# Optimization experiments

Measured on AMD Instinct MI355X. Metric: run time of the kernel, lower is better.

The kernel has to match this reference:

```python
import jax, jax.numpy as jnp
import numpy as np

N, E, D_IN, D_OUT, R = 50000, 800000, 128, 128, 8


def setup_inputs() -> dict:
    key = jax.random.key(0)
    ks = jax.random.split(key, 6)
    x = jax.random.normal(ks[0], (N, D_IN), dtype=jnp.float32)
    W_rel = jax.random.normal(ks[1], (R, D_IN, D_OUT), dtype=jnp.float32) * (1.0 / np.sqrt(D_IN))
    W_self_w = jax.random.normal(ks[2], (D_OUT, D_IN), dtype=jnp.float32) * (1.0 / np.sqrt(D_IN))
    W_self_b = jax.random.normal(ks[3], (D_OUT,), dtype=jnp.float32) * 0.01
    edge_index = jax.random.randint(ks[4], (2, E), 0, N, dtype=jnp.int32)
    edge_type = jax.random.randint(ks[5], (E,), 0, R, dtype=jnp.int32)
    return {"x": x, "W_rel": W_rel, "W_self_w": W_self_w, "W_self_b": W_self_b,
            "edge_index": edge_index, "edge_type": edge_type}


def reference(x, W_rel, W_self_w, W_self_b, edge_index, edge_type):
    n = x.shape[0]
    # self-loop linear (nn.Linear: y = x @ W.T + b)
    out = x @ W_self_w.T + W_self_b
    src = edge_index[0]
    dst = edge_index[1]
    # Per-relation transform of all nodes: h[r, n, :] = x[n] @ W_rel[r]
    # (mathematically identical to per-edge bmm(x[src], W_rel[rel]))
    h = jnp.einsum('nd,rdo->rno', x, W_rel)  # [R, N, D_OUT]
    msg = h[edge_type, src]                   # [E, D_OUT] gather
    agg = jax.ops.segment_sum(msg, dst, num_segments=n)  # scatter-add
    deg = jax.ops.segment_sum(jnp.ones_like(dst, dtype=x.dtype), dst, num_segments=n)
    deg = jnp.maximum(deg, 1.0)[:, None]
    out = jax.nn.relu(out + agg / deg)
    # dropout p=0.0 / eval mode -> identity
    return out
```

## Files before the change

### kernel.cpp

```cpp
#include <hip/hip_runtime.h>
#include <hip/hip_bf16.h>


#define D 128
#define RNUM 8
#define KREL (RNUM * D)
#define KTOT (KREL + D)
#define BLK_M 64

#define BSHIFT 6
#define BRANGE 64
#define BCAP   2048
#define NBKT_MAX 784
#define CSTRIDE 16

typedef short short8 __attribute__((ext_vector_type(8)));
typedef float float4v __attribute__((ext_vector_type(4)));
typedef float float2v __attribute__((ext_vector_type(2)));

static __device__ __forceinline__ unsigned int f2b(float f) {
    unsigned int u = __float_as_uint(f);
    return (u + 0x7fffu + ((u >> 16) & 1u)) >> 16;
}
static __device__ __forceinline__ float b2f_lo(unsigned int u) {
    return __uint_as_float(u << 16);
}
static __device__ __forceinline__ float b2f_hi(unsigned int u) {
    return __uint_as_float(u & 0xffff0000u);
}

static __device__ __forceinline__ void gl_lds16(const void* g, void* l) {
    __builtin_amdgcn_global_load_lds(
        (const __attribute__((address_space(1))) unsigned int*)g,
        (__attribute__((address_space(3))) unsigned int*)l, 16, 0, 0);
}

__global__ void prep_kernel(const float* __restrict__ x,
                            const float* __restrict__ W_rel,
                            const float* __restrict__ W_self,
                            unsigned short* __restrict__ xb,
                            unsigned short* __restrict__ Bt,
                            int* __restrict__ gcur,
                            int Nn, int xb_blocks, int bt_blocks, int gz) {
    if (blockIdx.x < (unsigned)xb_blocks) {
        int t = blockIdx.x * 256 + threadIdx.x;
        int n = t >> 5;
        int c = (t & 31) * 4;
        if (n >= Nn) return;
        float4 v = *(const float4*)(x + (size_t)n * D + c);
        unsigned int p0 = f2b(v.x) | (f2b(v.y) << 16);
        unsigned int p1 = f2b(v.z) | (f2b(v.w) << 16);
        *(uint2*)(xb + (size_t)n * D + c) = make_uint2(p0, p1);
    } else if (blockIdx.x < (unsigned)(xb_blocks + bt_blocks)) {
        int idx = (blockIdx.x - xb_blocks) * 256 + threadIdx.x;
        if (idx >= 128 * KTOT) return;
        int o = idx / KTOT;
        int k = idx - o * KTOT;
        float v = (k < KREL) ? W_rel[(size_t)k * D + o]
                             : W_self[(size_t)o * D + (k - KREL)];
        Bt[idx] = (unsigned short)f2b(v);
    } else {
        int idx = (blockIdx.x - xb_blocks - bt_blocks) * 256 + threadIdx.x;
        if (idx < gz) gcur[idx] = 0;
    }
}

__global__ __launch_bounds__(256) void coarse_kernel(
        const int* __restrict__ ei, const int* __restrict__ et,
        int* __restrict__ gcur, int* __restrict__ data, int E, int nbkt) {
    __shared__ int cnt[NBKT_MAX];
    int t = threadIdx.x;
    for (int i = t; i < nbkt; i += 256) cnt[i] = 0;
    __syncthreads();

    int rec[8], rb[8], rk[8];
    int e0 = blockIdx.x * 2048;
#pragma unroll
    for (int j = 0; j < 8; ++j) {
        int e = e0 + j * 256 + t;
        bool ok = e < E;
        int s = ok ? ei[e] : 0;
        int d = ok ? ei[E + e] : 0;
        int r = ok ? et[e] : 0;
        int bkt = d >> BSHIFT;
        rec[j] = s | ((d & (BRANGE - 1)) << 16) | (r << 22);
        rb[j] = ok ? bkt : -1;
        rk[j] = ok ? atomicAdd(&cnt[bkt], 1) : 0;
    }
    __syncthreads();

    for (int i = t; i < nbkt; i += 256) {
        int c = cnt[i];
        if (c) cnt[i] = i * BCAP + atomicAdd(&gcur[i * CSTRIDE], c);
    }
    __syncthreads();

#pragma unroll
    for (int j = 0; j < 8; ++j) {
        if (rb[j] >= 0) {
            int pos = cnt[rb[j]] + rk[j];
            if (pos < (rb[j] + 1) * BCAP)
                data[pos] = rec[j];
        }
    }
}

__global__ __launch_bounds__(256) void fine_kernel(
        int* __restrict__ data, const int* __restrict__ gcur,
        int* __restrict__ offsets, int* __restrict__ deg, int Nn) {
    __shared__ int recs[BCAP];
    __shared__ int hist[BRANGE * RNUM];
    int b = blockIdx.x;
    int t = threadIdx.x;
    int gbase = b * BCAP;
    int cnt = gcur[b * CSTRIDE];
    if (cnt > BCAP) cnt = BCAP;

    for (int i = t; i < BRANGE * RNUM; i += 256) hist[i] = 0;
    __syncthreads();

    for (int i = t; i < cnt; i += 256) {
        int rec = data[gbase + i];
        recs[i] = rec;
        int n = (rec >> 16) & (BRANGE - 1);
        int r = (rec >> 22) & 7;
        atomicAdd(&hist[n * RNUM + r], 1);
    }
    __syncthreads();

    if (t < BRANGE) {
        int dsum = 0;
#pragma unroll
        for (int r = 0; r < RNUM; ++r) dsum += hist[t * RNUM + r];
        int pad = (dsum + 7) & ~7;
        int x = pad;
        for (int off = 1; off < 64; off <<= 1) {
            int y = __shfl_up(x, off);
            if (t >= off) x += y;
        }
        int nb = gbase + (x - pad);
        int n0 = b * BRANGE + t;
        if (n0 < Nn) { offsets[n0] = nb; deg[n0] = dsum; }
        for (int i = dsum; i < pad; ++i)
            data[nb + i] = (int)0xF0000000u;
        int q = nb;
#pragma unroll
        for (int r = 0; r < RNUM; ++r) { int c = hist[t * RNUM + r]; hist[t * RNUM + r] = q; q += c; }
    }
    __syncthreads();

    for (int i = t; i < cnt; i += 256) {
        int rec = recs[i];
        int n = (rec >> 16) & (BRANGE - 1);
        int r = (rec >> 22) & 7;
        int pos = atomicAdd(&hist[n * RNUM + r], 1);
        data[pos] = (rec & 0xFFFF) | (r << 28);
    }
}

__global__ __launch_bounds__(256) void aggregate_kernel(
        const unsigned short* __restrict__ xb,
        const int* __restrict__ offsets,
        const int* __restrict__ deg,
        const int* __restrict__ sorted,
        unsigned short* __restrict__ A,
        int Nn) {
    int node = blockIdx.x * 4 + (threadIdx.x >> 6);
    if (node >= Nn) return;
    int lane = threadIdx.x & 63;
    int laneoff = lane * 2;

    int b0 = __builtin_amdgcn_readfirstlane(offsets[node]);
    int dg = __builtin_amdgcn_readfirstlane(deg[node]);
    int b1 = b0 + ((dg + 7) & ~7);
    float inv = 1.0f / fmaxf((float)dg, 1.0f);

    unsigned short* arow = A + (size_t)node * KREL + laneoff;

    unsigned wmask = 0;
    int cur = 8;
    float2v racc = {0.0f, 0.0f};

    for (int e = b0; e < b1; e += 8) {
        int pv[8];
#pragma unroll
        for (int j = 0; j < 8; ++j)
            pv[j] = __builtin_amdgcn_readfirstlane(sorted[e + j]);
        unsigned int u[8];
#pragma unroll
        for (int j = 0; j < 8; ++j)
            u[j] = *(const unsigned int*)(xb + (size_t)(pv[j] & 0x0FFFFFFF) * D + laneoff);
#pragma unroll
        for (int j = 0; j < 8; ++j) {
            int r = ((unsigned)pv[j]) >> 28;
            int si = (r < 8) ? r : 8;
            float2v f;
            f.x = b2f_lo(u[j]);
            f.y = b2f_hi(u[j]);
            if (si != cur) {
                if (cur < 8) {
                    *(unsigned int*)(arow + cur * D) =
                        f2b(racc.x * inv) | (f2b(racc.y * inv) << 16);
                    wmask |= 1u << cur;
                }
                cur = si;
                racc = f;
            } else {
                racc += f;
            }
        }
    }
    if (cur < 8) {
        *(unsigned int*)(arow + cur * D) =
            f2b(racc.x * inv) | (f2b(racc.y * inv) << 16);
        wmask |= 1u << cur;
    }
#pragma unroll
    for (int r = 0; r < 8; ++r)
        if (!(wmask & (1u << r)))
            *(unsigned int*)(arow + r * D) = 0u;
}

__global__ __launch_bounds__(256) void gemm_kernel(
        const unsigned short* __restrict__ A,
        const unsigned short* __restrict__ xb,
        const unsigned short* __restrict__ Bt,
        const float* __restrict__ bias,
        float* __restrict__ out,
        int Nn) {
    __shared__ unsigned short As[BLK_M * 32];
    __shared__ unsigned short Bs[128 * 32];

    const int tid  = threadIdx.x;
    const int lane = tid & 63;
    const int w    = tid >> 6;
    const int wm   = w & 1;
    const int wn   = w >> 1;
    const int l16  = lane & 15;
    const int q    = lane >> 4;
    const int row0 = blockIdx.x * BLK_M;

    float4v acc[2][4] = {};

    const int sr = lane >> 2;
    const int sc = (lane & 3) * 8;

    for (int kk = 0; kk < KTOT; kk += 32) {
        const unsigned short* abase;
        size_t apitch; int kof;
        if (kk < KREL) { abase = A;  apitch = KREL; kof = kk; }
        else           { abase = xb; apitch = D;    kof = kk - KREL; }
        {
            int r = w * 16 + sr;
            const unsigned short* g = abase + (size_t)(row0 + r) * apitch + kof + sc;
            gl_lds16(g, &As[w * 512]);
        }
#pragma unroll
        for (int p = 0; p < 2; ++p) {
            int r = w * 32 + p * 16 + sr;
            const unsigned short* g = Bt + (size_t)r * KTOT + kk + sc;
            gl_lds16(g, &Bs[(w * 2 + p) * 512]);
        }
        __syncthreads();

        short8 a[2], b[4];
#pragma unroll
        for (int mi = 0; mi < 2; ++mi)
            a[mi] = *reinterpret_cast<const short8*>(&As[(wm * 32 + mi * 16 + l16) * 32 + q * 8]);
#pragma unroll
        for (int ni = 0; ni < 4; ++ni)
            b[ni] = *reinterpret_cast<const short8*>(&Bs[(wn * 64 + ni * 16 + l16) * 32 + q * 8]);
#pragma unroll
        for (int mi = 0; mi < 2; ++mi)
#pragma unroll
            for (int ni = 0; ni < 4; ++ni)
                acc[mi][ni] = __builtin_amdgcn_mfma_f32_16x16x32_bf16(a[mi], b[ni], acc[mi][ni], 0, 0, 0);
        __syncthreads();
    }

#pragma unroll
    for (int ni = 0; ni < 4; ++ni) {
        int c = wn * 64 + ni * 16 + l16;
        float bv = bias[c];
#pragma unroll
        for (int mi = 0; mi < 2; ++mi) {
#pragma unroll
            for (int j = 0; j < 4; ++j) {
                int gr = row0 + wm * 32 + mi * 16 + q * 4 + j;
                if (gr < Nn)
                    out[(size_t)gr * D + c] = fmaxf(acc[mi][ni][j] + bv, 0.0f);
            }
        }
    }
}

extern "C" void kernel_launch(void* const* d_in, const int* in_sizes, int n_in,
                              void* d_out, int out_size, void* d_ws, size_t ws_size,
                              hipStream_t stream) {
    const float* x      = (const float*)d_in[0];
    const float* W_rel  = (const float*)d_in[1];
    const float* W_self = (const float*)d_in[2];
    const float* W_bias = (const float*)d_in[3];
    const int*   ei     = (const int*)d_in[4];
    const int*   et     = (const int*)d_in[5];

    const int Nn = in_sizes[0] / D;
    const int E  = in_sizes[4] / 2;
    const int npad = ((Nn + BLK_M - 1) / BLK_M) * BLK_M;
    const int nbkt = (Nn + BRANGE - 1) >> BSHIFT;
    const int gz   = nbkt * CSTRIDE;

    char* p = (char*)d_ws;
    auto take = [&](size_t bytes) { char* q = p; p += (bytes + 255) & ~(size_t)255; return q; };
    unsigned short* A    = (unsigned short*)take((size_t)npad * KREL * sizeof(unsigned short));
    unsigned short* xb   = (unsigned short*)take((size_t)npad * D * sizeof(unsigned short));
    unsigned short* Bt   = (unsigned short*)take((size_t)128 * KTOT * sizeof(unsigned short));
    int* offsets = (int*)take((size_t)Nn * sizeof(int));
    int* deg     = (int*)take((size_t)Nn * sizeof(int));
    int* gcur    = (int*)take((size_t)gz * sizeof(int));
    int* data    = (int*)take((size_t)nbkt * BCAP * sizeof(int));

    const int xb_blocks = (Nn * 32 + 255) / 256;
    const int bt_blocks = (128 * KTOT + 255) / 256;
    const int gz_blocks = (gz + 255) / 256;
    prep_kernel<<<xb_blocks + bt_blocks + gz_blocks, 256, 0, stream>>>(
        x, W_rel, W_self, xb, Bt, gcur, Nn, xb_blocks, bt_blocks, gz);
    coarse_kernel<<<(E + 2047) / 2048, 256, 0, stream>>>(ei, et, gcur, data, E, nbkt);
    fine_kernel<<<nbkt, 256, 0, stream>>>(data, gcur, offsets, deg, Nn);
    aggregate_kernel<<<(Nn + 3) / 4, 256, 0, stream>>>(xb, offsets, deg, data, A, Nn);
    gemm_kernel<<<npad / BLK_M, 256, 0, stream>>>(A, xb, Bt, W_bias, (float*)d_out, Nn);
}
```

Before: 204.3 us.

## Double-buffer GEMM LDS tiles with BK=64 and XOR-swizzled layout

Rewrites the GEMM main loop to use two LDS buffers with a K-tile of 64. The next tile is loaded while MFMAs run on the current one, and there is a single waitcnt plus barrier per iteration. An XOR swizzle on the 16-byte column chunk is meant to cut LDS bank conflicts on the fragment reads. The cost is four times the LDS footprint, which could lower occupancy.

```diff
diff --git a/kernel.cpp b/kernel.cpp
--- a/kernel.cpp
+++ b/kernel.cpp
@@ -7,6 +7,7 @@
 #define KREL (RNUM * D)
 #define KTOT (KREL + D)
 #define BLK_M 64
+#define BK 64
 
 #define BSHIFT 6
 #define BRANGE 64
@@ -228,8 +229,8 @@
         const float* __restrict__ bias,
         float* __restrict__ out,
         int Nn) {
-    __shared__ unsigned short As[BLK_M * 32];
-    __shared__ unsigned short Bs[128 * 32];
+    __shared__ unsigned short As[2][BLK_M * BK];
+    __shared__ unsigned short Bs[2][128 * BK];
 
     const int tid  = threadIdx.x;
     const int lane = tid & 63;
@@ -240,43 +241,79 @@
     const int q    = lane >> 4;
     const int row0 = blockIdx.x * BLK_M;
 
+    const int sr8 = lane >> 3;
+    const int sp  = (lane & 7) ^ sr8;
+
     float4v acc[2][4] = {};
 
-    const int sr = lane >> 2;
-    const int sc = (lane & 3) * 8;
-
-    for (int kk = 0; kk < KTOT; kk += 32) {
-        const unsigned short* abase;
-        size_t apitch; int kof;
-        if (kk < KREL) { abase = A;  apitch = KREL; kof = kk; }
-        else           { abase = xb; apitch = D;    kof = kk - KREL; }
-        {
-            int r = w * 16 + sr;
-            const unsigned short* g = abase + (size_t)(row0 + r) * apitch + kof + sc;
-            gl_lds16(g, &As[w * 512]);
-        }
-#pragma unroll
-        for (int p = 0; p < 2; ++p) {
-            int r = w * 32 + p * 16 + sr;
-            const unsigned short* g = Bt + (size_t)r * KTOT + kk + sc;
-            gl_lds16(g, &Bs[(w * 2 + p) * 512]);
-        }
-        __syncthreads();
-
-        short8 a[2], b[4];
-#pragma unroll
-        for (int mi = 0; mi < 2; ++mi)
-            a[mi] = *reinterpret_cast<const short8*>(&As[(wm * 32 + mi * 16 + l16) * 32 + q * 8]);
-#pragma unroll
-        for (int ni = 0; ni < 4; ++ni)
-            b[ni] = *reinterpret_cast<const short8*>(&Bs[(wn * 64 + ni * 16 + l16) * 32 + q * 8]);
-#pragma unroll
-        for (int mi = 0; mi < 2; ++mi)
-#pragma unroll
-            for (int ni = 0; ni < 4; ++ni)
-                acc[mi][ni] = __builtin_amdgcn_mfma_f32_16x16x32_bf16(a[mi], b[ni], acc[mi][ni], 0, 0, 0);
-        __syncthreads();
-    }
+#define STAGE(buf, kt)                                                          \
+    {                                                                           \
+        const int kk_ = (kt) * BK;                                              \
+        const unsigned short* abase_; size_t apitch_; int kof_;                 \
+        if (kk_ < KREL) { abase_ = A;  apitch_ = KREL; kof_ = kk_; }            \
+        else            { abase_ = xb; apitch_ = D;    kof_ = kk_ - KREL; }     \
+        _Pragma("unroll")                                                       \
+        for (int t_ = 0; t_ < 2; ++t_) {                                        \
+            int r_ = w * 16 + t_ * 8 + sr8;                                     \
+            const unsigned short* g_ =                                          \
+                abase_ + (size_t)(row0 + r_) * apitch_ + kof_ + sp * 8;         \
+            gl_lds16(g_, &As[buf][(w * 16 + t_ * 8) * BK]);                     \
+        }                                                                       \
+        _Pragma("unroll")                                                       \
+        for (int p_ = 0; p_ < 4; ++p_) {                                        \
+            int r_ = w * 32 + p_ * 8 + sr8;                                     \
+            const unsigned short* g_ = Bt + (size_t)r_ * KTOT + kk_ + sp * 8;   \
+            gl_lds16(g_, &Bs[buf][(w * 32 + p_ * 8) * BK]);                     \
+        }                                                                       \
+    }
+
+#define COMPUTE(buf)                                                            \
+    {                                                                           \
+        short8 a_[2][2], b_[2][4];                                              \
+        _Pragma("unroll")                                                       \
+        for (int ks_ = 0; ks_ < 2; ++ks_) {                                     \
+            _Pragma("unroll")                                                   \
+            for (int mi_ = 0; mi_ < 2; ++mi_) {                                 \
+                int r_ = wm * 32 + mi_ * 16 + l16;                              \
+                int c_ = (ks_ * 4 + q) ^ (l16 & 7);                             \
+                a_[ks_][mi_] = *reinterpret_cast<const short8*>(                \
+                    &As[buf][r_ * BK + c_ * 8]);                                \
+            }                                                                   \
+            _Pragma("unroll")                                                   \
+            for (int ni_ = 0; ni_ < 4; ++ni_) {                                 \
+                int r_ = wn * 64 + ni_ * 16 + l16;                              \
+                int c_ = (ks_ * 4 + q) ^ (l16 & 7);                             \
+                b_[ks_][ni_] = *reinterpret_cast<const short8*>(                \
+                    &Bs[buf][r_ * BK + c_ * 8]);                                \
+            }                                                                   \
+        }                                                                       \
+        _Pragma("unroll")                                                       \
+        for (int ks_ = 0; ks_ < 2; ++ks_)                                       \
+            _Pragma("unroll")                                                   \
+            for (int mi_ = 0; mi_ < 2; ++mi_)                                   \
+                _Pragma("unroll")                                               \
+                for (int ni_ = 0; ni_ < 4; ++ni_)                               \
+                    acc[mi_][ni_] = __builtin_amdgcn_mfma_f32_16x16x32_bf16(    \
+                        a_[ks_][mi_], b_[ks_][ni_], acc[mi_][ni_], 0, 0, 0);    \
+    }
+
+    STAGE(0, 0);
+    asm volatile("s_waitcnt vmcnt(0)" ::: "memory");
+    __builtin_amdgcn_s_barrier();
+
+    int buf = 0;
+    const int NT = KTOT / BK;
+    for (int kt = 0; kt < NT - 1; ++kt) {
+        STAGE(buf ^ 1, kt + 1);
+        COMPUTE(buf);
+        asm volatile("s_waitcnt vmcnt(0)" ::: "memory");
+        __builtin_amdgcn_s_barrier();
+        buf ^= 1;
+    }
+    COMPUTE(buf);
+
+#undef STAGE
+#undef COMPUTE
 
 #pragma unroll
     for (int ni = 0; ni < 4; ++ni) {
```

Measured after the change: 204.3 us. Within noise of the previous version (+0.0%).

## Fuse per-relation aggregation into GEMM via swizzled LDS A-tile

Applied to the files above, without the earlier changes.

Merges the aggregate and GEMM kernels. Each block of 32 nodes builds its full bf16 A row (8 relation means plus the self features) in a swizzled LDS tile, then runs MFMA directly against Bt read from global memory. This drops the round trip of the large intermediate A matrix through HBM and one kernel launch. In exchange, B is reloaded from global (L2) per block without LDS staging, the block tile shrinks to 32 rows, the 72KB LDS footprint limits occupancy, and gather latency now serializes with compute inside each block.

```diff
diff --git a/kernel.cpp b/kernel.cpp
--- a/kernel.cpp
+++ b/kernel.cpp
@@ -6,7 +6,8 @@
 #define RNUM 8
 #define KREL (RNUM * D)
 #define KTOT (KREL + D)
-#define BLK_M 64
+#define BLK_M 32
+#define ROWB (KTOT * 2)
 
 #define BSHIFT 6
 #define BRANGE 64
@@ -29,10 +30,11 @@
     return __uint_as_float(u & 0xffff0000u);
 }
 
-static __device__ __forceinline__ void gl_lds16(const void* g, void* l) {
-    __builtin_amdgcn_global_load_lds(
-        (const __attribute__((address_space(1))) unsigned int*)g,
-        (__attribute__((address_space(3))) unsigned int*)l, 16, 0, 0);
+static __device__ __forceinline__ int at4(int nl, int elem2) {
+    int byte = elem2 * 2;
+    int P = byte >> 4;
+    int Ps = (P & ~7) | ((P ^ nl) & 7);
+    return nl * ROWB + Ps * 16 + (byte & 15);
 }
 
 __global__ void prep_kernel(const float* __restrict__ x,
@@ -158,135 +160,124 @@
     }
 }
 
-__global__ __launch_bounds__(256) void aggregate_kernel(
+__global__ __launch_bounds__(256) void fused_kernel(
         const unsigned short* __restrict__ xb,
         const int* __restrict__ offsets,
         const int* __restrict__ deg,
         const int* __restrict__ sorted,
-        unsigned short* __restrict__ A,
-        int Nn) {
-    int node = blockIdx.x * 4 + (threadIdx.x >> 6);
-    if (node >= Nn) return;
-    int lane = threadIdx.x & 63;
-    int laneoff = lane * 2;
-
-    int b0 = __builtin_amdgcn_readfirstlane(offsets[node]);
-    int dg = __builtin_amdgcn_readfirstlane(deg[node]);
-    int b1 = b0 + ((dg + 7) & ~7);
-    float inv = 1.0f / fmaxf((float)dg, 1.0f);
-
-    unsigned short* arow = A + (size_t)node * KREL + laneoff;
-
-    unsigned wmask = 0;
-    int cur = 8;
-    float2v racc = {0.0f, 0.0f};
-
-    for (int e = b0; e < b1; e += 8) {
-        int pv[8];
-#pragma unroll
-        for (int j = 0; j < 8; ++j)
-            pv[j] = __builtin_amdgcn_readfirstlane(sorted[e + j]);
-        unsigned int u[8];
-#pragma unroll
-        for (int j = 0; j < 8; ++j)
-            u[j] = *(const unsigned int*)(xb + (size_t)(pv[j] & 0x0FFFFFFF) * D + laneoff);
-#pragma unroll
-        for (int j = 0; j < 8; ++j) {
-            int r = ((unsigned)pv[j]) >> 28;
-            int si = (r < 8) ? r : 8;
-            float2v f;
-            f.x = b2f_lo(u[j]);
-            f.y = b2f_hi(u[j]);
-            if (si != cur) {
-                if (cur < 8) {
-                    *(unsigned int*)(arow + cur * D) =
-                        f2b(racc.x * inv) | (f2b(racc.y * inv) << 16);
-                    wmask |= 1u << cur;
-                }
-                cur = si;
-                racc = f;
-            } else {
-                racc += f;
-            }
-        }
-    }
-    if (cur < 8) {
-        *(unsigned int*)(arow + cur * D) =
-            f2b(racc.x * inv) | (f2b(racc.y * inv) << 16);
-        wmask |= 1u << cur;
-    }
-#pragma unroll
-    for (int r = 0; r < 8; ++r)
-        if (!(wmask & (1u << r)))
-            *(unsigned int*)(arow + r * D) = 0u;
-}
-
-__global__ __launch_bounds__(256) void gemm_kernel(
-        const unsigned short* __restrict__ A,
-        const unsigned short* __restrict__ xb,
         const unsigned short* __restrict__ Bt,
         const float* __restrict__ bias,
         float* __restrict__ out,
         int Nn) {
-    __shared__ unsigned short As[BLK_M * 32];
-    __shared__ unsigned short Bs[128 * 32];
-
-    const int tid  = threadIdx.x;
-    const int lane = tid & 63;
-    const int w    = tid >> 6;
-    const int wm   = w & 1;
-    const int wn   = w >> 1;
-    const int l16  = lane & 15;
-    const int q    = lane >> 4;
-    const int row0 = blockIdx.x * BLK_M;
-
-    float4v acc[2][4] = {};
-
-    const int sr = lane >> 2;
-    const int sc = (lane & 3) * 8;
-
-    for (int kk = 0; kk < KTOT; kk += 32) {
-        const unsigned short* abase;
-        size_t apitch; int kof;
-        if (kk < KREL) { abase = A;  apitch = KREL; kof = kk; }
-        else           { abase = xb; apitch = D;    kof = kk - KREL; }
-        {
-            int r = w * 16 + sr;
-            const unsigned short* g = abase + (size_t)(row0 + r) * apitch + kof + sc;
-            gl_lds16(g, &As[w * 512]);
-        }
-#pragma unroll
-        for (int p = 0; p < 2; ++p) {
-            int r = w * 32 + p * 16 + sr;
-            const unsigned short* g = Bt + (size_t)r * KTOT + kk + sc;
-            gl_lds16(g, &Bs[(w * 2 + p) * 512]);
-        }
-        __syncthreads();
-
-        short8 a[2], b[4];
-#pragma unroll
-        for (int mi = 0; mi < 2; ++mi)
-            a[mi] = *reinterpret_cast<const short8*>(&As[(wm * 32 + mi * 16 + l16) * 32 + q * 8]);
-#pragma unroll
-        for (int ni = 0; ni < 4; ++ni)
-            b[ni] = *reinterpret_cast<const short8*>(&Bs[(wn * 64 + ni * 16 + l16) * 32 + q * 8]);
-#pragma unroll
-        for (int mi = 0; mi < 2; ++mi)
-#pragma unroll
-            for (int ni = 0; ni < 4; ++ni)
-                acc[mi][ni] = __builtin_amdgcn_mfma_f32_16x16x32_bf16(a[mi], b[ni], acc[mi][ni], 0, 0, 0);
-        __syncthreads();
-    }
-
-#pragma unroll
-    for (int ni = 0; ni < 4; ++ni) {
-        int c = wn * 64 + ni * 16 + l16;
+    __shared__ unsigned short At[BLK_M * KTOT];
+
+    const int tid   = threadIdx.x;
+    const int lane  = tid & 63;
+    const int w     = tid >> 6;
+    const int node0 = blockIdx.x * BLK_M;
+    const int laneoff = lane * 2;
+
+    for (int i = 0; i < 8; ++i) {
+        int node = node0 + w * 8 + i;
+        if (node >= Nn) break;
+        int nl = w * 8 + i;
+
+        int b0 = __builtin_amdgcn_readfirstlane(offsets[node]);
+        int dg = __builtin_amdgcn_readfirstlane(deg[node]);
+        int b1 = b0 + ((dg + 7) & ~7);
+        float inv = 1.0f / fmaxf((float)dg, 1.0f);
+
+        unsigned wmask = 0;
+        int cur = 8;
+        float2v racc = {0.0f, 0.0f};
+
+        for (int e = b0; e < b1; e += 8) {
+            int pv[8];
+#pragma unroll
+            for (int j = 0; j < 8; ++j)
+                pv[j] = __builtin_amdgcn_readfirstlane(sorted[e + j]);
+            unsigned int u[8];
+#pragma unroll
+            for (int j = 0; j < 8; ++j)
+                u[j] = *(const unsigned int*)(xb + (size_t)(pv[j] & 0x0FFFFFFF) * D + laneoff);
+#pragma unroll
+            for (int j = 0; j < 8; ++j) {
+                int r = ((unsigned)pv[j]) >> 28;
+                int si = (r < 8) ? r : 8;
+                float2v f;
+                f.x = b2f_lo(u[j]);
+                f.y = b2f_hi(u[j]);
+                if (si != cur) {
+                    if (cur < 8) {
+                        *(unsigned int*)((char*)At + at4(nl, cur * D + laneoff)) =
+                            f2b(racc.x * inv) | (f2b(racc.y * inv) << 16);
+                        wmask |= 1u << cur;
+                    }
+                    cur = si;
+                    racc = f;
+                } else {
+                    racc += f;
+                }
+            }
+        }
+        if (cur < 8) {
+            *(unsigned int*)((char*)At + at4(nl, cur * D + laneoff)) =
+                f2b(racc.x * inv) | (f2b(racc.y * inv) << 16);
+            wmask |= 1u << cur;
+        }
+#pragma unroll
+        for (int r = 0; r < 8; ++r)
+            if (!(wmask & (1u << r)))
+                *(unsigned int*)((char*)At + at4(nl, r * D + laneoff)) = 0u;
+        unsigned int us = *(const unsigned int*)(xb + (size_t)node * D + laneoff);
+        *(unsigned int*)((char*)At + at4(nl, KREL + laneoff)) = us;
+    }
+    __syncthreads();
+
+    const int l16 = lane & 15;
+    const int q   = lane >> 4;
+    const int nc0 = w * 32;
+
+    float4v acc[2][2] = {};
+
+#pragma unroll
+    for (int t = 0; t < KTOT / 64; ++t) {
+        const int kk = t * 64;
+        short8 a[2][2], b[2][2];
+#pragma unroll
+        for (int ks = 0; ks < 2; ++ks) {
+            int c = ks * 4 + q;
+#pragma unroll
+            for (int mi = 0; mi < 2; ++mi) {
+                int r_ = mi * 16 + l16;
+                a[ks][mi] = *(const short8*)((const char*)At +
+                    r_ * ROWB + kk * 2 + ((c ^ (r_ & 7)) << 4));
+            }
+#pragma unroll
+            for (int ni = 0; ni < 2; ++ni) {
+                int o = nc0 + ni * 16 + l16;
+                b[ks][ni] = *(const short8*)(Bt + (size_t)o * KTOT + kk + c * 8);
+            }
+        }
+#pragma unroll
+        for (int ks = 0; ks < 2; ++ks)
+#pragma unroll
+            for (int mi = 0; mi < 2; ++mi)
+#pragma unroll
+                for (int ni = 0; ni < 2; ++ni)
+                    acc[mi][ni] = __builtin_amdgcn_mfma_f32_16x16x32_bf16(
+                        a[ks][mi], b[ks][ni], acc[mi][ni], 0, 0, 0);
+    }
+
+#pragma unroll
+    for (int ni = 0; ni < 2; ++ni) {
+        int c = nc0 + ni * 16 + l16;
         float bv = bias[c];
 #pragma unroll
         for (int mi = 0; mi < 2; ++mi) {
 #pragma unroll
             for (int j = 0; j < 4; ++j) {
-                int gr = row0 + wm * 32 + mi * 16 + q * 4 + j;
+                int gr = node0 + mi * 16 + q * 4 + j;
                 if (gr < Nn)
                     out[(size_t)gr * D + c] = fmaxf(acc[mi][ni][j] + bv, 0.0f);
             }
@@ -306,14 +297,13 @@
 
     const int Nn = in_sizes[0] / D;
     const int E  = in_sizes[4] / 2;
-    const int npad = ((Nn + BLK_M - 1) / BLK_M) * BLK_M;
     const int nbkt = (Nn + BRANGE - 1) >> BSHIFT;
     const int gz   = nbkt * CSTRIDE;
+    const int nblk = (Nn + BLK_M - 1) / BLK_M;
 
     char* p = (char*)d_ws;
     auto take = [&](size_t bytes) { char* q = p; p += (bytes + 255) & ~(size_t)255; return q; };
-    unsigned short* A    = (unsigned short*)take((size_t)npad * KREL * sizeof(unsigned short));
-    unsigned short* xb   = (unsigned short*)take((size_t)npad * D * sizeof(unsigned short));
+    unsigned short* xb   = (unsigned short*)take((size_t)Nn * D * sizeof(unsigned short));
     unsigned short* Bt   = (unsigned short*)take((size_t)128 * KTOT * sizeof(unsigned short));
     int* offsets = (int*)take((size_t)Nn * sizeof(int));
     int* deg     = (int*)take((size_t)Nn * sizeof(int));
@@ -327,6 +317,6 @@
         x, W_rel, W_self, xb, Bt, gcur, Nn, xb_blocks, bt_blocks, gz);
     coarse_kernel<<<(E + 2047) / 2048, 256, 0, stream>>>(ei, et, gcur, data, E, nbkt);
     fine_kernel<<<nbkt, 256, 0, stream>>>(data, gcur, offsets, deg, Nn);
-    aggregate_kernel<<<(Nn + 3) / 4, 256, 0, stream>>>(xb, offsets, deg, data, A, Nn);
-    gemm_kernel<<<npad / BLK_M, 256, 0, stream>>>(A, xb, Bt, W_bias, (float*)d_out, Nn);
-}
+    fused_kernel<<<nblk, 256, 0, stream>>>(xb, offsets, deg, data, Bt, W_bias,
+                                           (float*)d_out, Nn);
+}
```

Measured after the change: 273.1 us. +33.7%, slower.

## Load GEMM operands directly from global into registers, dropping LDS staging

Applied to the files above, without the earlier changes.

The GEMM kernel no longer stages A and B tiles through shared memory with global_load_lds and two barriers per K-step. Each wave now loads its MFMA fragments straight from global memory into registers, two K-substeps at a time, with the K loop fully unrolled. This removes barrier and LDS round-trip overhead but gives up operand sharing across waves, so each wave fetches B and A redundantly through L1/L2. It also raises register pressure.

```diff
diff --git a/kernel.cpp b/kernel.cpp
--- a/kernel.cpp
+++ b/kernel.cpp
@@ -27,12 +27,6 @@
 }
 static __device__ __forceinline__ float b2f_hi(unsigned int u) {
     return __uint_as_float(u & 0xffff0000u);
-}
-
-static __device__ __forceinline__ void gl_lds16(const void* g, void* l) {
-    __builtin_amdgcn_global_load_lds(
-        (const __attribute__((address_space(1))) unsigned int*)g,
-        (__attribute__((address_space(3))) unsigned int*)l, 16, 0, 0);
 }
 
 __global__ void prep_kernel(const float* __restrict__ x,
@@ -228,9 +222,6 @@
         const float* __restrict__ bias,
         float* __restrict__ out,
         int Nn) {
-    __shared__ unsigned short As[BLK_M * 32];
-    __shared__ unsigned short Bs[128 * 32];
-
     const int tid  = threadIdx.x;
     const int lane = tid & 63;
     const int w    = tid >> 6;
@@ -242,40 +233,34 @@
 
     float4v acc[2][4] = {};
 
-    const int sr = lane >> 2;
-    const int sc = (lane & 3) * 8;
-
-    for (int kk = 0; kk < KTOT; kk += 32) {
-        const unsigned short* abase;
-        size_t apitch; int kof;
-        if (kk < KREL) { abase = A;  apitch = KREL; kof = kk; }
-        else           { abase = xb; apitch = D;    kof = kk - KREL; }
-        {
-            int r = w * 16 + sr;
-            const unsigned short* g = abase + (size_t)(row0 + r) * apitch + kof + sc;
-            gl_lds16(g, &As[w * 512]);
-        }
-#pragma unroll
-        for (int p = 0; p < 2; ++p) {
-            int r = w * 32 + p * 16 + sr;
-            const unsigned short* g = Bt + (size_t)r * KTOT + kk + sc;
-            gl_lds16(g, &Bs[(w * 2 + p) * 512]);
-        }
-        __syncthreads();
-
-        short8 a[2], b[4];
-#pragma unroll
-        for (int mi = 0; mi < 2; ++mi)
-            a[mi] = *reinterpret_cast<const short8*>(&As[(wm * 32 + mi * 16 + l16) * 32 + q * 8]);
-#pragma unroll
-        for (int ni = 0; ni < 4; ++ni)
-            b[ni] = *reinterpret_cast<const short8*>(&Bs[(wn * 64 + ni * 16 + l16) * 32 + q * 8]);
-#pragma unroll
-        for (int mi = 0; mi < 2; ++mi)
+    const unsigned short* a0 = A  + (size_t)(row0 + wm * 32 + l16) * KREL + q * 8;
+    const unsigned short* x0 = xb + (size_t)(row0 + wm * 32 + l16) * D    + q * 8;
+    const unsigned short* bp = Bt + (size_t)(wn * 64 + l16) * KTOT       + q * 8;
+
+#pragma unroll
+    for (int t = 0; t < KTOT / 64; ++t) {
+        const int kk = t * 64;
+        short8 a[2][2], b[2][4];
+#pragma unroll
+        for (int ks = 0; ks < 2; ++ks) {
+            const int ko = kk + ks * 32;
+#pragma unroll
+            for (int mi = 0; mi < 2; ++mi)
+                a[ks][mi] = (kk < KREL)
+                    ? *(const short8*)(a0 + (size_t)mi * 16 * KREL + ko)
+                    : *(const short8*)(x0 + (size_t)mi * 16 * D + (ko - KREL));
 #pragma unroll
             for (int ni = 0; ni < 4; ++ni)
-                acc[mi][ni] = __builtin_amdgcn_mfma_f32_16x16x32_bf16(a[mi], b[ni], acc[mi][ni], 0, 0, 0);
-        __syncthreads();
+                b[ks][ni] = *(const short8*)(bp + (size_t)ni * 16 * KTOT + ko);
+        }
+#pragma unroll
+        for (int ks = 0; ks < 2; ++ks)
+#pragma unroll
+            for (int mi = 0; mi < 2; ++mi)
+#pragma unroll
+                for (int ni = 0; ni < 4; ++ni)
+                    acc[mi][ni] = __builtin_amdgcn_mfma_f32_16x16x32_bf16(
+                        a[ks][mi], b[ks][ni], acc[mi][ni], 0, 0, 0);
     }
 
 #pragma unroll
```

Result: slower. 262.6 us (+28.5%).
